# Kernel tuning notes

Measured on AMD Instinct MI355X. Metric: run time of the kernel, lower is better.

## Reference

```python
import math
import jax, jax.numpy as jnp
import numpy as np

B, S, D, K = 64, 512, 4096, 8
COND_H, SIG_F, SIG_H = 256, 128, 256


def setup_inputs() -> dict:
    key = jax.random.key(0)
    ks = jax.random.split(key, 12)
    emb = jax.random.normal(ks[0], (B, S, D), dtype=jnp.float32)
    seqlens = jax.random.randint(ks[1], (B,), 0, S - K, dtype=jnp.int64)
    timesteps = jax.random.uniform(ks[2], (B,), dtype=jnp.float32)
    # cond_mlp: Linear(D, COND_H) -> GELU -> Linear(COND_H, K*D)
    W1 = jax.random.normal(ks[3], (D, COND_H), dtype=jnp.float32) / np.sqrt(D)
    b1 = jax.random.normal(ks[4], (COND_H,), dtype=jnp.float32) * 0.01
    W2 = jax.random.normal(ks[5], (COND_H, K * D), dtype=jnp.float32) / np.sqrt(COND_H)
    b2 = jax.random.normal(ks[6], (K * D,), dtype=jnp.float32) * 0.01
    # sigma_mlp: Linear(SIG_F, SIG_H) -> SiLU -> Linear(SIG_H, K*D)
    sW1 = jax.random.normal(ks[7], (SIG_F, SIG_H), dtype=jnp.float32) / np.sqrt(SIG_F)
    sb1 = jax.random.normal(ks[8], (SIG_H,), dtype=jnp.float32) * 0.01
    sW2 = jax.random.normal(ks[9], (SIG_H, K * D), dtype=jnp.float32) / np.sqrt(SIG_H)
    sb2 = jax.random.normal(ks[10], (K * D,), dtype=jnp.float32) * 0.01
    return {"crossattn_emb": emb, "crossattn_seqlens": seqlens, "timesteps": timesteps,
            "W1": W1, "b1": b1, "W2": W2, "b2": b2,
            "sW1": sW1, "sb1": sb1, "sW2": sW2, "sb2": sb2}


def _sigma_features(t):
    # sinusoidal features over sigma, dim SIG_F (half cos, half sin)
    half = SIG_F // 2
    freqs = jnp.exp(-math.log(10000.0) * jnp.arange(half, dtype=jnp.float32) / half)
    ang = t.astype(jnp.float32)[:, None] * freqs[None, :]  # [B, half]
    return jnp.concatenate([jnp.cos(ang), jnp.sin(ang)], axis=-1)  # [B, SIG_F]


def reference(crossattn_emb, crossattn_seqlens, timesteps,
              W1, b1, W2, b2, sW1, sb1, sW2, sb2):
    b, s, d = crossattn_emb.shape
    # masked mean-pool over content slots
    pos = jnp.arange(s)[None, :]
    mask = (pos < crossattn_seqlens[:, None]).astype(crossattn_emb.dtype)  # [B,S]
    denom = jnp.clip(jnp.sum(mask, axis=1, keepdims=True), 1.0)
    pooled = jnp.einsum('bsd,bs->bd', crossattn_emb, mask) / denom  # [B,D]
    # cond MLP (exact GELU, matching torch nn.GELU default)
    h = jax.nn.gelu(pooled @ W1 + b1, approximate=False)
    postfix = (h @ W2 + b2).reshape(b, K, d)
    # sigma-conditional residual
    sh = jax.nn.silu(_sigma_features(timesteps) @ sW1 + sb1)
    postfix = postfix + (sh @ sW2 + sb2).reshape(b, K, d)
    # front_of_padding splice: overwrite [seqlen, seqlen+K) per sample
    offsets = crossattn_seqlens[:, None] + jnp.arange(K)[None, :]  # [B,K]
    return crossattn_emb.at[jnp.arange(b)[:, None], offsets].set(postfix)
```

## Files before the change

kernel.cpp:

```cpp
#include <hip/hip_runtime.h>
#include <math.h>

#define BB 64
#define SS 512
#define DD 4096
#define KK 8
#define COND_H 256
#define SIG_F 128
#define SIG_H 256
#define KD (KK*DD)
#define SCHUNKS 8
#define SROWS (SS/SCHUNKS)
#define KSLICES 32
#define KSL (DD/KSLICES)

__device__ inline bool seql_is64(const int* sq) {
    bool is64 = true;
#pragma unroll
    for (int i = 1; i < 64; i += 2) is64 &= (sq[i] == 0);
    return is64;
}
__device__ inline int load_seqlen(const int* sq, int b, bool is64) {
    return is64 ? sq[2 * b] : sq[b];
}

__global__ __launch_bounds__(256) void k_copy_pool(
        const float* __restrict__ emb, const int* __restrict__ seql_raw,
        float* __restrict__ out, float* __restrict__ partial) {
    const int dchunk = blockIdx.x;
    const int sy     = blockIdx.y;
    const int b      = blockIdx.z;
    const int tid    = threadIdx.x;
    const int d0     = dchunk * 1024 + tid * 4;

    const bool is64 = seql_is64(seql_raw);
    const int  sl   = load_seqlen(seql_raw, b, is64);

    size_t base = ((size_t)b * SS + (size_t)sy * SROWS) * DD + d0;
    float4 sum = make_float4(0.f, 0.f, 0.f, 0.f);

    const int s0 = sy * SROWS;
#pragma unroll 4
    for (int i = 0; i < SROWS; ++i) {
        float4 v = *(const float4*)(emb + base);
        *(float4*)(out + base) = v;
        if (s0 + i < sl) {
            sum.x += v.x; sum.y += v.y; sum.z += v.z; sum.w += v.w;
        }
        base += DD;
    }
    size_t pidx = ((size_t)sy * BB + b) * DD + d0;
    *(float4*)(partial + pidx) = sum;
}

__global__ __launch_bounds__(256) void k_cond_l1(
        const float* __restrict__ partial, const int* __restrict__ seql_raw,
        const float* __restrict__ W1, float* __restrict__ ph) {
    __shared__ float pooled[8][KSL];
    const int ks  = blockIdx.x;
    const int bg  = blockIdx.y;
    const int tid = threadIdx.x;

    const bool is64 = seql_is64(seql_raw);

#pragma unroll
    for (int e = 0; e < 4; ++e) {
        int idx = e * 256 + tid;
        int b8  = idx >> 7;
        int d   = idx & (KSL - 1);
        int b   = bg * 8 + b8;
        float s = 0.f;
        size_t col = (size_t)ks * KSL + d;
#pragma unroll
        for (int sy = 0; sy < SCHUNKS; ++sy)
            s += partial[((size_t)sy * BB + b) * DD + col];
        float denom = fmaxf((float)load_seqlen(seql_raw, b, is64), 1.0f);
        pooled[b8][d] = s / denom;
    }
    __syncthreads();

    float acc[8];
#pragma unroll
    for (int i = 0; i < 8; ++i) acc[i] = 0.f;
#pragma unroll 8
    for (int k = 0; k < KSL; ++k) {
        float w = W1[((size_t)ks * KSL + k) * COND_H + tid];
#pragma unroll
        for (int b8 = 0; b8 < 8; ++b8)
            acc[b8] = fmaf(pooled[b8][k], w, acc[b8]);
    }
#pragma unroll
    for (int b8 = 0; b8 < 8; ++b8)
        ph[((size_t)ks * BB + bg * 8 + b8) * COND_H + tid] = acc[b8];
}

__global__ __launch_bounds__(256) void k_l1_finish(
        const float* __restrict__ ph, const float* __restrict__ b1,
        const float* __restrict__ tsteps,
        const float* __restrict__ sW1, const float* __restrict__ sb1,
        float* __restrict__ h_ws, float* __restrict__ sh_ws) {
    __shared__ float lds[SIG_F];
    const int tid = threadIdx.x;

    if (blockIdx.x < BB) {
        const int b = blockIdx.x;
        float acc = b1[tid];
#pragma unroll 8
        for (int ks = 0; ks < KSLICES; ++ks)
            acc += ph[((size_t)ks * BB + b) * COND_H + tid];
        float g = 0.5f * acc * (1.0f + erff(acc * 0.70710678118654752f));
        h_ws[b * COND_H + tid] = g;
    } else {
        const int b = blockIdx.x - BB;
        if (tid < SIG_F / 2) {
            float t = tsteps[b];
            float fr = expf(-9.210340371976184f * (float)tid * (1.0f / 64.0f));
            float ang = t * fr;
            lds[tid]      = cosf(ang);
            lds[tid + 64] = sinf(ang);
        }
        __syncthreads();
        float acc = sb1[tid];
#pragma unroll 8
        for (int c = 0; c < SIG_F; ++c)
            acc = fmaf(lds[c], sW1[c * SIG_H + tid], acc);
        float s = acc / (1.0f + expf(-acc));
        sh_ws[b * SIG_H + tid] = s;
    }
}

__global__ __launch_bounds__(256) void k_layer2_splice(
        const float* __restrict__ h_ws, const float* __restrict__ sh_ws,
        const float* __restrict__ W2, const float* __restrict__ b2,
        const float* __restrict__ sW2, const float* __restrict__ sb2,
        const int* __restrict__ seql_raw, float* __restrict__ out) {
    __shared__ float hl[BB * COND_H];
    const int tid = threadIdx.x;
    const int tj  = tid & 15;
    const int bg  = tid >> 4;
    const int j   = blockIdx.x * 64 + tj * 4;

    float acc[4][4];
#pragma unroll
    for (int i = 0; i < 4; ++i)
#pragma unroll
        for (int q = 0; q < 4; ++q) acc[i][q] = 0.0f;

    for (int pass = 0; pass < 2; ++pass) {
        const float* Hs = pass ? sh_ws : h_ws;
        const float* Wm = pass ? sW2 : W2;
        __syncthreads();
#pragma unroll
        for (int i = 0; i < 16; ++i) {
            int idx = (i * 256 + tid) * 4;
            *(float4*)&hl[idx] = *(const float4*)&Hs[idx];
        }
        __syncthreads();

        for (int c4 = 0; c4 < COND_H / 4; ++c4) {
            float wf[4][4];
#pragma unroll
            for (int cc = 0; cc < 4; ++cc) {
                float4 w = *(const float4*)&Wm[(size_t)(c4 * 4 + cc) * KD + j];
                wf[cc][0] = w.x; wf[cc][1] = w.y; wf[cc][2] = w.z; wf[cc][3] = w.w;
            }
#pragma unroll
            for (int b4 = 0; b4 < 4; ++b4) {
                const float4 hv = *(const float4*)&hl[(bg * 4 + b4) * COND_H + c4 * 4];
#pragma unroll
                for (int jj = 0; jj < 4; ++jj) {
                    float a = acc[b4][jj];
                    a = fmaf(hv.x, wf[0][jj], a);
                    a = fmaf(hv.y, wf[1][jj], a);
                    a = fmaf(hv.z, wf[2][jj], a);
                    a = fmaf(hv.w, wf[3][jj], a);
                    acc[b4][jj] = a;
                }
            }
        }
    }

    float4 bb = *(const float4*)&b2[j];
    float4 sb = *(const float4*)&sb2[j];
    bb.x += sb.x; bb.y += sb.y; bb.z += sb.z; bb.w += sb.w;

    const int k = j >> 12;
    const int d = j & (DD - 1);
    const bool is64 = seql_is64(seql_raw);
#pragma unroll
    for (int b4 = 0; b4 < 4; ++b4) {
        const int b = bg * 4 + b4;
        const int sl = load_seqlen(seql_raw, b, is64);
        size_t o = ((size_t)b * SS + (size_t)(sl + k)) * DD + d;
        float4 v;
        v.x = acc[b4][0] + bb.x;
        v.y = acc[b4][1] + bb.y;
        v.z = acc[b4][2] + bb.z;
        v.w = acc[b4][3] + bb.w;
        *(float4*)&out[o] = v;
    }
}

extern "C" void kernel_launch(void* const* d_in, const int* in_sizes, int n_in,
                              void* d_out, int out_size, void* d_ws, size_t ws_size,
                              hipStream_t stream) {
    const float* emb    = (const float*)d_in[0];
    const int*   seql   = (const int*)  d_in[1];
    const float* tsteps = (const float*)d_in[2];
    const float* W1     = (const float*)d_in[3];
    const float* b1     = (const float*)d_in[4];
    const float* W2     = (const float*)d_in[5];
    const float* b2     = (const float*)d_in[6];
    const float* sW1    = (const float*)d_in[7];
    const float* sb1    = (const float*)d_in[8];
    const float* sW2    = (const float*)d_in[9];
    const float* sb2    = (const float*)d_in[10];
    float* out = (float*)d_out;

    const size_t PART_FLOATS = (size_t)SCHUNKS * BB * DD;
    const size_t PH_FLOATS   = (size_t)KSLICES * BB * COND_H;
    float* partial = (float*)d_ws;
    float* ph      = partial + PART_FLOATS;
    float* h_ws    = ph + PH_FLOATS;
    float* sh_ws   = h_ws + (size_t)BB * COND_H;

    hipLaunchKernelGGL(k_copy_pool, dim3(4, 8, 64), dim3(256), 0, stream,
                       emb, seql, out, partial);
    hipLaunchKernelGGL(k_cond_l1, dim3(KSLICES, 8), dim3(256), 0, stream,
                       partial, seql, W1, ph);
    hipLaunchKernelGGL(k_l1_finish, dim3(128), dim3(256), 0, stream,
                       ph, b1, tsteps, sW1, sb1, h_ws, sh_ws);
    hipLaunchKernelGGL(k_layer2_splice, dim3(512), dim3(256), 0, stream,
                       h_ws, sh_ws, W2, b2, sW2, sb2, seql, out);
}
```

Before: 272.3 us.

## Use nontemporal copy, split layer-1 wider, batch sigma MLP, pad LDS in layer 2

The bulk copy-and-pool kernel now uses nontemporal loads and stores so the streamed embedding does not pollute caches. Layer-1 is split across 64 K-slices instead of 32 for more parallelism. The sigma MLP moves into the layer-1 kernel and handles 8 samples per block so weight loads are reused. Layer-2 loads both activation matrices into padded LDS once, removing the mid-kernel reload and barrier, at the cost of twice the LDS footprint and possibly lower occupancy.

```diff
diff --git a/kernel.cpp b/kernel.cpp
--- a/kernel.cpp
+++ b/kernel.cpp
@@ -11,8 +11,17 @@
 #define KD (KK*DD)
 #define SCHUNKS 8
 #define SROWS (SS/SCHUNKS)
-#define KSLICES 32
+#define KSLICES 64
 #define KSL (DD/KSLICES)
+#define PADC 260
+
+typedef float f32x4 __attribute__((ext_vector_type(4)));
+__device__ inline f32x4 nt_load4(const float* p) {
+    return __builtin_nontemporal_load((const f32x4*)p);
+}
+__device__ inline void nt_store4(float* p, f32x4 v) {
+    __builtin_nontemporal_store(v, (f32x4*)p);
+}
 
 __device__ inline bool seql_is64(const int* sq) {
     bool is64 = true;
@@ -37,96 +46,107 @@
     const int  sl   = load_seqlen(seql_raw, b, is64);
 
     size_t base = ((size_t)b * SS + (size_t)sy * SROWS) * DD + d0;
-    float4 sum = make_float4(0.f, 0.f, 0.f, 0.f);
+    f32x4 sum = {0.f, 0.f, 0.f, 0.f};
 
     const int s0 = sy * SROWS;
 #pragma unroll 4
     for (int i = 0; i < SROWS; ++i) {
-        float4 v = *(const float4*)(emb + base);
-        *(float4*)(out + base) = v;
-        if (s0 + i < sl) {
-            sum.x += v.x; sum.y += v.y; sum.z += v.z; sum.w += v.w;
-        }
+        f32x4 v = nt_load4(emb + base);
+        nt_store4(out + base, v);
+        if (s0 + i < sl) sum += v;
         base += DD;
     }
     size_t pidx = ((size_t)sy * BB + b) * DD + d0;
-    *(float4*)(partial + pidx) = sum;
-}
-
-__global__ __launch_bounds__(256) void k_cond_l1(
+    *(f32x4*)(partial + pidx) = sum;
+}
+
+__global__ __launch_bounds__(256) void k_l1_split(
         const float* __restrict__ partial, const int* __restrict__ seql_raw,
-        const float* __restrict__ W1, float* __restrict__ ph) {
-    __shared__ float pooled[8][KSL];
-    const int ks  = blockIdx.x;
-    const int bg  = blockIdx.y;
+        const float* __restrict__ W1, const float* __restrict__ tsteps,
+        const float* __restrict__ sW1, const float* __restrict__ sb1,
+        float* __restrict__ ph, float* __restrict__ sh_ws) {
+    __shared__ float smem[8][SIG_F];
     const int tid = threadIdx.x;
 
-    const bool is64 = seql_is64(seql_raw);
-
-#pragma unroll
-    for (int e = 0; e < 4; ++e) {
-        int idx = e * 256 + tid;
-        int b8  = idx >> 7;
-        int d   = idx & (KSL - 1);
-        int b   = bg * 8 + b8;
-        float s = 0.f;
-        size_t col = (size_t)ks * KSL + d;
-#pragma unroll
-        for (int sy = 0; sy < SCHUNKS; ++sy)
-            s += partial[((size_t)sy * BB + b) * DD + col];
-        float denom = fmaxf((float)load_seqlen(seql_raw, b, is64), 1.0f);
-        pooled[b8][d] = s / denom;
-    }
-    __syncthreads();
-
-    float acc[8];
-#pragma unroll
-    for (int i = 0; i < 8; ++i) acc[i] = 0.f;
+    if (blockIdx.x < 512) {
+        const int ks = blockIdx.x >> 3;
+        const int bg = blockIdx.x & 7;
+        const bool is64 = seql_is64(seql_raw);
+
+#pragma unroll
+        for (int e = 0; e < 2; ++e) {
+            int idx = e * 256 + tid;
+            int b8  = idx >> 6;
+            int d   = idx & (KSL - 1);
+            int b   = bg * 8 + b8;
+            float s = 0.f;
+            size_t col = (size_t)ks * KSL + d;
+#pragma unroll
+            for (int sy = 0; sy < SCHUNKS; ++sy)
+                s += partial[((size_t)sy * BB + b) * DD + col];
+            float denom = fmaxf((float)load_seqlen(seql_raw, b, is64), 1.0f);
+            smem[b8][d] = s / denom;
+        }
+        __syncthreads();
+
+        float acc[8];
+#pragma unroll
+        for (int i = 0; i < 8; ++i) acc[i] = 0.f;
 #pragma unroll 8
-    for (int k = 0; k < KSL; ++k) {
-        float w = W1[((size_t)ks * KSL + k) * COND_H + tid];
+        for (int k = 0; k < KSL; ++k) {
+            float w = W1[((size_t)ks * KSL + k) * COND_H + tid];
+#pragma unroll
+            for (int b8 = 0; b8 < 8; ++b8)
+                acc[b8] = fmaf(smem[b8][k], w, acc[b8]);
+        }
 #pragma unroll
         for (int b8 = 0; b8 < 8; ++b8)
-            acc[b8] = fmaf(pooled[b8][k], w, acc[b8]);
-    }
-#pragma unroll
-    for (int b8 = 0; b8 < 8; ++b8)
-        ph[((size_t)ks * BB + bg * 8 + b8) * COND_H + tid] = acc[b8];
+            ph[((size_t)ks * BB + bg * 8 + b8) * COND_H + tid] = acc[b8];
+    } else {
+        const int sb = blockIdx.x - 512;
+#pragma unroll
+        for (int e = 0; e < 4; ++e) {
+            int idx = e * 256 + tid;
+            int b8  = idx >> 7;
+            int f   = idx & 127;
+            float t = tsteps[sb * 8 + b8];
+            int fi = (f < 64) ? f : (f - 64);
+            float fr = expf(-0.14391156831213413f * (float)fi);
+            float ang = t * fr;
+            smem[b8][f] = (f < 64) ? cosf(ang) : sinf(ang);
+        }
+        __syncthreads();
+
+        float acc[8];
+#pragma unroll
+        for (int i = 0; i < 8; ++i) acc[i] = sb1[tid];
+#pragma unroll 8
+        for (int c = 0; c < SIG_F; ++c) {
+            float w = sW1[c * SIG_H + tid];
+#pragma unroll
+            for (int b8 = 0; b8 < 8; ++b8)
+                acc[b8] = fmaf(smem[b8][c], w, acc[b8]);
+        }
+#pragma unroll
+        for (int b8 = 0; b8 < 8; ++b8) {
+            float a = acc[b8];
+            float s = a / (1.0f + expf(-a));
+            sh_ws[(sb * 8 + b8) * SIG_H + tid] = s;
+        }
+    }
 }
 
 __global__ __launch_bounds__(256) void k_l1_finish(
         const float* __restrict__ ph, const float* __restrict__ b1,
-        const float* __restrict__ tsteps,
-        const float* __restrict__ sW1, const float* __restrict__ sb1,
-        float* __restrict__ h_ws, float* __restrict__ sh_ws) {
-    __shared__ float lds[SIG_F];
+        float* __restrict__ h_ws) {
+    const int b = blockIdx.x;
     const int tid = threadIdx.x;
-
-    if (blockIdx.x < BB) {
-        const int b = blockIdx.x;
-        float acc = b1[tid];
+    float acc = b1[tid];
 #pragma unroll 8
-        for (int ks = 0; ks < KSLICES; ++ks)
-            acc += ph[((size_t)ks * BB + b) * COND_H + tid];
-        float g = 0.5f * acc * (1.0f + erff(acc * 0.70710678118654752f));
-        h_ws[b * COND_H + tid] = g;
-    } else {
-        const int b = blockIdx.x - BB;
-        if (tid < SIG_F / 2) {
-            float t = tsteps[b];
-            float fr = expf(-9.210340371976184f * (float)tid * (1.0f / 64.0f));
-            float ang = t * fr;
-            lds[tid]      = cosf(ang);
-            lds[tid + 64] = sinf(ang);
-        }
-        __syncthreads();
-        float acc = sb1[tid];
-#pragma unroll 8
-        for (int c = 0; c < SIG_F; ++c)
-            acc = fmaf(lds[c], sW1[c * SIG_H + tid], acc);
-        float s = acc / (1.0f + expf(-acc));
-        sh_ws[b * SIG_H + tid] = s;
-    }
+    for (int ks = 0; ks < KSLICES; ++ks)
+        acc += ph[((size_t)ks * BB + b) * COND_H + tid];
+    float g = 0.5f * acc * (1.0f + erff(acc * 0.70710678118654752f));
+    h_ws[b * COND_H + tid] = g;
 }
 
 __global__ __launch_bounds__(256) void k_layer2_splice(
@@ -134,12 +154,23 @@
         const float* __restrict__ W2, const float* __restrict__ b2,
         const float* __restrict__ sW2, const float* __restrict__ sb2,
         const int* __restrict__ seql_raw, float* __restrict__ out) {
-    __shared__ float hl[BB * COND_H];
+    __shared__ float hl[BB][PADC];
+    __shared__ float sl_[BB][PADC];
     const int tid = threadIdx.x;
     const int tj  = tid & 15;
     const int bg  = tid >> 4;
     const int j   = blockIdx.x * 64 + tj * 4;
 
+#pragma unroll
+    for (int e = 0; e < 16; ++e) {
+        int idx = e * 256 + tid;
+        int row = idx >> 6;
+        int c4i = idx & 63;
+        *(float4*)&hl[row][c4i * 4]  = *(const float4*)&h_ws[row * COND_H + c4i * 4];
+        *(float4*)&sl_[row][c4i * 4] = *(const float4*)&sh_ws[row * COND_H + c4i * 4];
+    }
+    __syncthreads();
+
     float acc[4][4];
 #pragma unroll
     for (int i = 0; i < 4; ++i)
@@ -147,16 +178,9 @@
         for (int q = 0; q < 4; ++q) acc[i][q] = 0.0f;
 
     for (int pass = 0; pass < 2; ++pass) {
-        const float* Hs = pass ? sh_ws : h_ws;
-        const float* Wm = pass ? sW2 : W2;
-        __syncthreads();
-#pragma unroll
-        for (int i = 0; i < 16; ++i) {
-            int idx = (i * 256 + tid) * 4;
-            *(float4*)&hl[idx] = *(const float4*)&Hs[idx];
-        }
-        __syncthreads();
-
+        const float* __restrict__ Wm = pass ? sW2 : W2;
+        const float (*A)[PADC] = pass ? sl_ : hl;
+#pragma unroll 2
         for (int c4 = 0; c4 < COND_H / 4; ++c4) {
             float wf[4][4];
 #pragma unroll
@@ -166,14 +190,14 @@
             }
 #pragma unroll
             for (int b4 = 0; b4 < 4; ++b4) {
-                const float4 hv = *(const float4*)&hl[(bg * 4 + b4) * COND_H + c4 * 4];
+                const float4 av = *(const float4*)&A[bg * 4 + b4][c4 * 4];
 #pragma unroll
                 for (int jj = 0; jj < 4; ++jj) {
                     float a = acc[b4][jj];
-                    a = fmaf(hv.x, wf[0][jj], a);
-                    a = fmaf(hv.y, wf[1][jj], a);
-                    a = fmaf(hv.z, wf[2][jj], a);
-                    a = fmaf(hv.w, wf[3][jj], a);
+                    a = fmaf(av.x, wf[0][jj], a);
+                    a = fmaf(av.y, wf[1][jj], a);
+                    a = fmaf(av.z, wf[2][jj], a);
+                    a = fmaf(av.w, wf[3][jj], a);
                     acc[b4][jj] = a;
                 }
             }
@@ -226,10 +250,10 @@
 
     hipLaunchKernelGGL(k_copy_pool, dim3(4, 8, 64), dim3(256), 0, stream,
                        emb, seql, out, partial);
-    hipLaunchKernelGGL(k_cond_l1, dim3(KSLICES, 8), dim3(256), 0, stream,
-                       partial, seql, W1, ph);
-    hipLaunchKernelGGL(k_l1_finish, dim3(128), dim3(256), 0, stream,
-                       ph, b1, tsteps, sW1, sb1, h_ws, sh_ws);
+    hipLaunchKernelGGL(k_l1_split, dim3(520), dim3(256), 0, stream,
+                       partial, seql, W1, tsteps, sW1, sb1, ph, sh_ws);
+    hipLaunchKernelGGL(k_l1_finish, dim3(64), dim3(256), 0, stream,
+                       ph, b1, h_ws);
     hipLaunchKernelGGL(k_layer2_splice, dim3(512), dim3(256), 0, stream,
                        h_ws, sh_ws, W2, b2, sW2, sb2, seql, out);
 }
```

Result: faster. 263.9 us (median of 2 runs) (-3.1%).
